# Kernel tuning notes

Hardware: AMD Instinct MI355X
Metric: run time of the kernel (lower is better)

The kernel has to match this reference:

```python
import jax, jax.numpy as jnp
import numpy as np

HIDDEN = 384
HEADS = 8
DIM_HEAD = HIDDEN // HEADS  # 48
INNER = DIM_HEAD * HEADS
SCALE = DIM_HEAD ** -0.5


def setup_inputs() -> dict:
    key = jax.random.key(0)
    k1, k2, k3, k4 = jax.random.split(key, 4)
    B, C, D, H, W = 2, HIDDEN, 16, 16, 8
    x = jax.random.normal(k1, (B, C, D, H, W), dtype=jnp.float32)
    # nn.Linear weights (stored as [out, in] in torch; use [in, out] here)
    w_qkv = jax.random.normal(k2, (C, 3 * INNER), dtype=jnp.float32) * (C ** -0.5)
    w_out = jax.random.normal(k3, (INNER, C), dtype=jnp.float32) * (INNER ** -0.5)
    b_out = jax.random.normal(k4, (C,), dtype=jnp.float32) * 0.02
    return {"x": x, "w_qkv": w_qkv, "w_out": w_out, "b_out": b_out}


def reference(x, w_qkv, w_out, b_out):
    B, C, D, H, W = x.shape
    N = D * H * W
    tokens = x.reshape(B, C, N).transpose(0, 2, 1)          # [B, N, C]
    qkv = tokens @ w_qkv                                     # [B, N, 3*inner]
    qkv = qkv.reshape(B, N, 3, HEADS, DIM_HEAD).transpose(2, 0, 3, 1, 4)
    q, k, v = qkv[0], qkv[1], qkv[2]                         # [B, h, N, dh]
    q = jnp.clip(q, -5.0, 5.0)
    k = jnp.clip(k, -5.0, 5.0)
    logits = jnp.einsum('bhnd,bhmd->bhnm', q, k) * SCALE     # [B, h, N, N]
    logits = logits - jnp.max(logits, axis=-1, keepdims=True)
    attn = jax.nn.softmax(logits, axis=-1)
    out = jnp.einsum('bhnm,bhmd->bhnd', attn, v)             # [B, h, N, dh]
    out = out.transpose(0, 2, 1, 3).reshape(B, N, INNER)     # [B, N, inner]
    out = out @ w_out + b_out                                # [B, N, C]
    out = out.transpose(0, 2, 1).reshape(B, C, D, H, W)
    return x + out
```

## Files before the change

### kernel.cpp

```cpp
#include <hip/hip_runtime.h>

#define B_SZ 2
#define C_IN 384
#define N_TOK 2048
#define HEADS 8
#define DH 48
#define J3 1152
#define ATTN_SCALE 0.14433756729740643f
#define KSPLIT 4
#define KEYS_PER_SPLIT 512

typedef __attribute__((ext_vector_type(8))) _Float16 f16x8;
typedef __attribute__((ext_vector_type(4))) _Float16 f16x4;
typedef __attribute__((ext_vector_type(4))) float f32x4;

__device__ __forceinline__ unsigned short f2h(float f) {
  _Float16 h = (_Float16)f;
  return __builtin_bit_cast(unsigned short, h);
}
__device__ __forceinline__ uint pk2(float a, float b) {
  return __builtin_bit_cast(uint, __builtin_amdgcn_cvt_pkrtz(a, b));
}

__global__ __launch_bounds__(256) void tr_kernel(
    const float* __restrict__ x, const float* __restrict__ wq,
    const float* __restrict__ wo, unsigned short* __restrict__ xh,
    unsigned short* __restrict__ wqh, unsigned short* __restrict__ woh) {
  const int z = blockIdx.z;
  const float* src;
  unsigned short* dst;
  int C;
  if (z < 2) {
    src = x + (size_t)z * C_IN * N_TOK;
    dst = xh + (size_t)z * N_TOK * C_IN;
    C = N_TOK;
  } else if (z == 2) {
    src = wq; dst = wqh; C = J3;
  } else {
    src = wo; dst = woh; C = C_IN;
  }
  const int c0 = blockIdx.x * 64;
  const int r0 = blockIdx.y * 64;
  if (c0 >= C) return;
  __shared__ unsigned short T[64][74];
  const int tid = threadIdx.x;
  const int cc = tid & 63;
#pragma unroll
  for (int i = 0; i < 16; ++i) {
    const int rr = 4 * i + (tid >> 6);
    T[cc][rr] = f2h(src[(size_t)(r0 + rr) * C + c0 + cc]);
  }
  __syncthreads();
  const int cc2 = tid >> 2;
  const int seg = (tid & 3) * 16;
  uint v[8];
#pragma unroll
  for (int k = 0; k < 8; ++k)
    v[k] = (uint)T[cc2][seg + 2 * k] | ((uint)T[cc2][seg + 2 * k + 1] << 16);
  unsigned short* dp = dst + (size_t)(c0 + cc2) * C_IN + r0 + seg;
  *(uint4*)dp = make_uint4(v[0], v[1], v[2], v[3]);
  *(uint4*)(dp + 8) = make_uint4(v[4], v[5], v[6], v[7]);
}

__global__ __launch_bounds__(256) void qkv_mfma(
    const unsigned short* __restrict__ xh, const unsigned short* __restrict__ wqh,
    unsigned short* __restrict__ Qo, unsigned short* __restrict__ Ko,
    unsigned short* __restrict__ Vo) {
  __shared__ __align__(16) unsigned short Ts[128][72];
  __shared__ __align__(16) unsigned short Ws[64][72];
  const int tid = threadIdx.x;
  const int w = tid >> 6, lane = tid & 63;
  const int lc = lane & 15, lg = lane >> 4;
  const int m0 = blockIdx.x * 128;
  const int j0 = blockIdx.y * 64;
  const int b = m0 >> 11;

  f32x4 acc[2][4];
#pragma unroll
  for (int i = 0; i < 2; ++i)
#pragma unroll
    for (int j = 0; j < 4; ++j) acc[i][j] = (f32x4){0.f, 0.f, 0.f, 0.f};

  const int trow = tid & 127, tseg = tid >> 7;
  const int wrow = tid & 63,  wseg = tid >> 6;

  for (int kk = 0; kk < C_IN; kk += 64) {
    {
      const uint4* s = (const uint4*)(xh + (size_t)(m0 + trow) * C_IN + kk + tseg * 32);
      uint4* d = (uint4*)&Ts[trow][tseg * 32];
      d[0] = s[0]; d[1] = s[1]; d[2] = s[2]; d[3] = s[3];
      const uint4* s2 = (const uint4*)(wqh + (size_t)(j0 + wrow) * C_IN + kk + wseg * 16);
      uint4* d2 = (uint4*)&Ws[wrow][wseg * 16];
      d2[0] = s2[0]; d2[1] = s2[1];
    }
    __syncthreads();
    f16x8 a[2][2], bf[4][2];
#pragma unroll
    for (int mt = 0; mt < 2; ++mt)
#pragma unroll
      for (int kh = 0; kh < 2; ++kh)
        a[mt][kh] = *(const f16x8*)&Ts[32 * w + 16 * mt + lc][32 * kh + 8 * lg];
#pragma unroll
    for (int jt = 0; jt < 4; ++jt)
#pragma unroll
      for (int kh = 0; kh < 2; ++kh)
        bf[jt][kh] = *(const f16x8*)&Ws[16 * jt + lc][32 * kh + 8 * lg];
#pragma unroll
    for (int mt = 0; mt < 2; ++mt)
#pragma unroll
      for (int jt = 0; jt < 4; ++jt)
#pragma unroll
        for (int kh = 0; kh < 2; ++kh)
          acc[mt][jt] = __builtin_amdgcn_mfma_f32_16x16x32_f16(a[mt][kh], bf[jt][kh], acc[mt][jt], 0, 0, 0);
    __syncthreads();
  }

#pragma unroll
  for (int jt = 0; jt < 4; ++jt) {
    const int jlo = j0 + 16 * jt;
    const int which = jlo / 384;
    const int rr = jlo - which * 384;
    const int head = rr / DH;
    const int dbase = rr - head * DH;
    const int d = dbase + lc;
    const int bh = b * HEADS + head;
#pragma unroll
    for (int mt = 0; mt < 2; ++mt)
#pragma unroll
      for (int r = 0; r < 4; ++r) {
        const int n = (m0 + 32 * w + 16 * mt + 4 * lg + r) & 2047;
        float val = acc[mt][jt][r];
        if (which == 0) {
          val = fminf(fmaxf(val, -5.f), 5.f) * ATTN_SCALE;
          Qo[((size_t)bh * N_TOK + n) * DH + d] = f2h(val);
        } else if (which == 1) {
          val = fminf(fmaxf(val, -5.f), 5.f);
          Ko[((size_t)bh * N_TOK + n) * DH + d] = f2h(val);
        } else {
          Vo[((size_t)bh * DH + d) * N_TOK + n] = f2h(val);
        }
      }
  }
}

__global__ __launch_bounds__(512) void attn_kernel(
    const unsigned short* __restrict__ Q, const unsigned short* __restrict__ K,
    const unsigned short* __restrict__ Vt, unsigned short* __restrict__ Opart,
    float2* __restrict__ ml) {
  const int qt = blockIdx.x, bh = blockIdx.y, ks = blockIdx.z;
  const int b = bh >> 3, h = bh & 7;
  const int n0 = qt * 128;
  const int tid = threadIdx.x;
  const int w = tid >> 6, lane = tid & 63;
  const int lc = lane & 15, lg = lane >> 4;

  __shared__ __align__(16) unsigned short Ks[2][64][56];
  __shared__ __align__(16) unsigned short Vs[2][48][68];

  const unsigned short* Qrow = Q + ((size_t)bh * N_TOK + n0 + 16 * w + lc) * DH;
  const f16x8 qf0 = *(const f16x8*)(Qrow + 8 * lg);
  f16x8 qf1 = {0, 0, 0, 0, 0, 0, 0, 0};
  {
    const f16x4 t = *(const f16x4*)(Qrow + 32 + 4 * lg);
    qf1[0] = t[0]; qf1[1] = t[1]; qf1[2] = t[2]; qf1[3] = t[3];
  }

  const unsigned short* Kg = K + (size_t)bh * N_TOK * DH + (size_t)ks * KEYS_PER_SPLIT * DH;
  const uint* Vg32 = (const uint*)(Vt + (size_t)bh * DH * N_TOK) + ks * (KEYS_PER_SPLIT / 2);

  uint kr[3], vr[3];
  auto issue = [&](int t0) {
    const uint* Ksrc = (const uint*)(Kg + (size_t)t0 * DH);
#pragma unroll
    for (int i = 0; i < 3; ++i) {
      const int dw = tid + i * 512;
      kr[i] = Ksrc[dw];
      vr[i] = Vg32[(size_t)(dw >> 5) * 1024 + (t0 >> 1) + (dw & 31)];
    }
  };
  auto commit = [&](int buf) {
#pragma unroll
    for (int i = 0; i < 3; ++i) {
      const int dw = tid + i * 512;
      const int key = dw / 24, c = dw - key * 24;
      *(uint*)&Ks[buf][key][2 * c] = kr[i];
      *(uint*)&Vs[buf][dw >> 5][2 * (dw & 31)] = vr[i];
    }
  };

  float m_run = -1e30f, l_run = 0.f;
  f32x4 oacc[3] = {{0,0,0,0},{0,0,0,0},{0,0,0,0}};

  issue(0);
  commit(0);

  for (int t = 0; t < KEYS_PER_SPLIT / 64; ++t) {
    const int cur = t & 1;
    if (t < KEYS_PER_SPLIT / 64 - 1) issue((t + 1) * 64);
    __syncthreads();

    f32x4 sac[4];
    __builtin_amdgcn_s_setprio(1);
#pragma unroll
    for (int it = 0; it < 4; ++it) {
      const int krow = 16 * it + lc;
      const f16x8 kf0 = *(const f16x8*)&Ks[cur][krow][8 * lg];
      f16x8 kf1 = {0, 0, 0, 0, 0, 0, 0, 0};
      const f16x4 tt = *(const f16x4*)&Ks[cur][krow][32 + 4 * lg];
      kf1[0] = tt[0]; kf1[1] = tt[1]; kf1[2] = tt[2]; kf1[3] = tt[3];
      const f32x4 z = {0.f, 0.f, 0.f, 0.f};
      f32x4 s = __builtin_amdgcn_mfma_f32_16x16x32_f16(kf0, qf0, z, 0, 0, 0);
      sac[it]  = __builtin_amdgcn_mfma_f32_16x16x32_f16(kf1, qf1, s, 0, 0, 0);
    }
    __builtin_amdgcn_s_setprio(0);

    float mt = -1e30f;
#pragma unroll
    for (int it = 0; it < 4; ++it)
#pragma unroll
      for (int r = 0; r < 4; ++r) mt = fmaxf(mt, sac[it][r]);
    mt = fmaxf(mt, __shfl_xor(mt, 16, 64));
    mt = fmaxf(mt, __shfl_xor(mt, 32, 64));
    const float mn = fmaxf(m_run, mt);
    const float rs = __expf(m_run - mn);
    m_run = mn;
    float p[4][4];
    float ps = 0.f;
#pragma unroll
    for (int it = 0; it < 4; ++it)
#pragma unroll
      for (int r = 0; r < 4; ++r) {
        p[it][r] = __expf(sac[it][r] - mn);
        ps += p[it][r];
      }
    ps += __shfl_xor(ps, 16, 64);
    ps += __shfl_xor(ps, 32, 64);
    l_run = l_run * rs + ps;
#pragma unroll
    for (int itd = 0; itd < 3; ++itd)
#pragma unroll
      for (int r = 0; r < 4; ++r) oacc[itd][r] *= rs;

    f16x8 pt[2];
#pragma unroll
    for (int ks2 = 0; ks2 < 2; ++ks2) {
      union { f16x8 v; uint u[4]; } pu;
      pu.u[0] = pk2(p[2 * ks2][0], p[2 * ks2][1]);
      pu.u[1] = pk2(p[2 * ks2][2], p[2 * ks2][3]);
      pu.u[2] = pk2(p[2 * ks2 + 1][0], p[2 * ks2 + 1][1]);
      pu.u[3] = pk2(p[2 * ks2 + 1][2], p[2 * ks2 + 1][3]);
      pt[ks2] = pu.v;
    }

    __builtin_amdgcn_s_setprio(1);
#pragma unroll
    for (int itd = 0; itd < 3; ++itd) {
      const int drow = 16 * itd + lc;
#pragma unroll
      for (int ks2 = 0; ks2 < 2; ++ks2) {
        const f16x4 v0 = *(const f16x4*)&Vs[cur][drow][4 * lg + 32 * ks2];
        const f16x4 v1 = *(const f16x4*)&Vs[cur][drow][4 * lg + 32 * ks2 + 16];
        f16x8 vf;
        vf[0] = v0[0]; vf[1] = v0[1]; vf[2] = v0[2]; vf[3] = v0[3];
        vf[4] = v1[0]; vf[5] = v1[1]; vf[6] = v1[2]; vf[7] = v1[3];
        oacc[itd] = __builtin_amdgcn_mfma_f32_16x16x32_f16(vf, pt[ks2], oacc[itd], 0, 0, 0);
      }
    }
    __builtin_amdgcn_s_setprio(0);

    if (t < KEYS_PER_SPLIT / 64 - 1) commit(cur ^ 1);
  }

  if (lg == 0)
    ml[(size_t)(ks * 16 + bh) * N_TOK + n0 + 16 * w + lc] = make_float2(m_run, l_run);
  unsigned short* Ap = Opart +
      ((size_t)(ks * B_SZ + b) * N_TOK + n0 + 16 * w + lc) * 384 + h * DH;
#pragma unroll
  for (int itd = 0; itd < 3; ++itd) {
    uint2 pkv;
    pkv.x = pk2(oacc[itd][0], oacc[itd][1]);
    pkv.y = pk2(oacc[itd][2], oacc[itd][3]);
    *(uint2*)(Ap + 16 * itd + 4 * lg) = pkv;
  }
}

__global__ __launch_bounds__(256) void combine_kernel(
    const unsigned short* __restrict__ Opart, const float2* __restrict__ ml,
    unsigned short* __restrict__ AOh) {
  const int vid = blockIdx.x * 256 + threadIdx.x;
  const int c8 = vid % 48;
  const int n  = (vid / 48) & 2047;
  const int b  = vid / (48 * 2048);
  const int c0 = c8 * 8;
  const int h  = c0 / 48;
  const int bh = b * 8 + h;
  const size_t PS = (size_t)B_SZ * N_TOK * 384;
  float2 e0 = ml[(size_t)(0 * 16 + bh) * N_TOK + n];
  float2 e1 = ml[(size_t)(1 * 16 + bh) * N_TOK + n];
  float2 e2 = ml[(size_t)(2 * 16 + bh) * N_TOK + n];
  float2 e3 = ml[(size_t)(3 * 16 + bh) * N_TOK + n];
  const float M = fmaxf(fmaxf(e0.x, e1.x), fmaxf(e2.x, e3.x));
  const float w0 = __expf(e0.x - M), w1 = __expf(e1.x - M);
  const float w2 = __expf(e2.x - M), w3 = __expf(e3.x - M);
  const float inv = 1.f / (w0 * e0.y + w1 * e1.y + w2 * e2.y + w3 * e3.y);
  const float s0 = w0 * inv, s1 = w1 * inv, s2 = w2 * inv, s3 = w3 * inv;
  const size_t o = ((size_t)b * N_TOK + n) * 384 + c0;
  union U8 { uint4 q; _Float16 e[8]; } u0, u1, u2, u3, r;
  u0.q = *(const uint4*)(Opart + 0 * PS + o);
  u1.q = *(const uint4*)(Opart + 1 * PS + o);
  u2.q = *(const uint4*)(Opart + 2 * PS + o);
  u3.q = *(const uint4*)(Opart + 3 * PS + o);
#pragma unroll
  for (int k = 0; k < 8; k += 2) {
    const float a = (float)u0.e[k] * s0 + (float)u1.e[k] * s1 +
                    (float)u2.e[k] * s2 + (float)u3.e[k] * s3;
    const float bb = (float)u0.e[k + 1] * s0 + (float)u1.e[k + 1] * s1 +
                     (float)u2.e[k + 1] * s2 + (float)u3.e[k + 1] * s3;
    *(uint*)&r.e[k] = pk2(a, bb);
  }
  *(uint4*)(AOh + o) = r.q;
}

__global__ __launch_bounds__(256) void proj_mfma(
    const unsigned short* __restrict__ AOh, const unsigned short* __restrict__ woh,
    const float* __restrict__ b_out, const float* __restrict__ x,
    float* __restrict__ out) {
  __shared__ __align__(16) unsigned short As[64][72];
  __shared__ __align__(16) unsigned short Bs[128][72];
  const int tid = threadIdx.x;
  const int w = tid >> 6, lane = tid & 63;
  const int lc = lane & 15, lg = lane >> 4;
  const int c0 = blockIdx.x * 64;
  const int m0 = blockIdx.y * 128;
  const int b = m0 >> 11;

  f32x4 acc[4][2];
#pragma unroll
  for (int i = 0; i < 4; ++i)
#pragma unroll
    for (int j = 0; j < 2; ++j) acc[i][j] = (f32x4){0.f, 0.f, 0.f, 0.f};

  const int arow = tid & 63,  aseg = tid >> 6;
  const int brow = tid & 127, bseg = tid >> 7;

  for (int kk = 0; kk < C_IN; kk += 64) {
    {
      const uint4* s = (const uint4*)(woh + (size_t)(c0 + arow) * C_IN + kk + aseg * 16);
      uint4* d = (uint4*)&As[arow][aseg * 16];
      d[0] = s[0]; d[1] = s[1];
      const uint4* s2 = (const uint4*)(AOh + (size_t)(m0 + brow) * C_IN + kk + bseg * 32);
      uint4* d2 = (uint4*)&Bs[brow][bseg * 32];
      d2[0] = s2[0]; d2[1] = s2[1]; d2[2] = s2[2]; d2[3] = s2[3];
    }
    __syncthreads();
    f16x8 a[4][2], bf[2][2];
#pragma unroll
    for (int ct = 0; ct < 4; ++ct)
#pragma unroll
      for (int kh = 0; kh < 2; ++kh)
        a[ct][kh] = *(const f16x8*)&As[16 * ct + lc][32 * kh + 8 * lg];
#pragma unroll
    for (int mt = 0; mt < 2; ++mt)
#pragma unroll
      for (int kh = 0; kh < 2; ++kh)
        bf[mt][kh] = *(const f16x8*)&Bs[32 * w + 16 * mt + lc][32 * kh + 8 * lg];
#pragma unroll
    for (int ct = 0; ct < 4; ++ct)
#pragma unroll
      for (int mt = 0; mt < 2; ++mt)
#pragma unroll
        for (int kh = 0; kh < 2; ++kh)
          acc[ct][mt] = __builtin_amdgcn_mfma_f32_16x16x32_f16(a[ct][kh], bf[mt][kh], acc[ct][mt], 0, 0, 0);
    __syncthreads();
  }

#pragma unroll
  for (int ct = 0; ct < 4; ++ct)
#pragma unroll
    for (int r = 0; r < 4; ++r) {
      const int c = c0 + 16 * ct + 4 * lg + r;
      const float bias = b_out[c];
#pragma unroll
      for (int mt = 0; mt < 2; ++mt) {
        const int n = (m0 + 32 * w + 16 * mt + lc) & 2047;
        const size_t off = ((size_t)b * C_IN + c) * N_TOK + n;
        out[off] = x[off] + bias + acc[ct][mt][r];
      }
    }
}

extern "C" void kernel_launch(void* const* d_in, const int* in_sizes, int n_in,
                              void* d_out, int out_size, void* d_ws, size_t ws_size,
                              hipStream_t stream) {
  const float* x     = (const float*)d_in[0];
  const float* w_qkv = (const float*)d_in[1];
  const float* w_out = (const float*)d_in[2];
  const float* b_out = (const float*)d_in[3];
  float* out = (float*)d_out;

  char* ws = (char*)d_ws;
  unsigned short* xh    = (unsigned short*)(ws);
  unsigned short* wqh   = (unsigned short*)(ws + 3145728);
  unsigned short* woh   = (unsigned short*)(ws + 4030464);
  unsigned short* Qb    = (unsigned short*)(ws + 4325376);
  unsigned short* Kb    = (unsigned short*)(ws + 7471104);
  unsigned short* Vb    = (unsigned short*)(ws + 10616832);
  unsigned short* Opart = (unsigned short*)(ws + 13762560);
  float2*         mlb   = (float2*)(ws + 26345472);
  unsigned short* AOh   = (unsigned short*)(ws + 27394048);

  tr_kernel<<<dim3(32, 6, 4), 256, 0, stream>>>(x, w_qkv, w_out, xh, wqh, woh);
  qkv_mfma<<<dim3(32, 18), 256, 0, stream>>>(xh, wqh, Qb, Kb, Vb);
  attn_kernel<<<dim3(16, 16, KSPLIT), 512, 0, stream>>>(Qb, Kb, Vb, Opart, mlb);
  combine_kernel<<<dim3(768), 256, 0, stream>>>(Opart, mlb, AOh);
  proj_mfma<<<dim3(6, 32), 256, 0, stream>>>(AOh, woh, b_out, x, out);
}
```

Before: 79.07 us.

## Use exp2 softmax with deferred rescale and coalesced V-transpose stores

```diff
diff --git a/kernel.cpp b/kernel.cpp
--- a/kernel.cpp
+++ b/kernel.cpp
@@ -6,9 +6,10 @@
 #define HEADS 8
 #define DH 48
 #define J3 1152
-#define ATTN_SCALE 0.14433756729740643f
+#define QSCALE_LOG2 0.20823509110768f
 #define KSPLIT 4
 #define KEYS_PER_SPLIT 512
+#define DEFER_THR 11.0f
 
 typedef __attribute__((ext_vector_type(8))) _Float16 f16x8;
 typedef __attribute__((ext_vector_type(4))) _Float16 f16x4;
@@ -20,6 +21,9 @@
 }
 __device__ __forceinline__ uint pk2(float a, float b) {
   return __builtin_bit_cast(uint, __builtin_amdgcn_cvt_pkrtz(a, b));
+}
+__device__ __forceinline__ float exp2g(float x) {
+  return __builtin_amdgcn_exp2f(x);
 }
 
 __global__ __launch_bounds__(256) void tr_kernel(
@@ -115,31 +119,53 @@
     __syncthreads();
   }
 
-#pragma unroll
-  for (int jt = 0; jt < 4; ++jt) {
-    const int jlo = j0 + 16 * jt;
-    const int which = jlo / 384;
-    const int rr = jlo - which * 384;
-    const int head = rr / DH;
-    const int dbase = rr - head * DH;
-    const int d = dbase + lc;
-    const int bh = b * HEADS + head;
-#pragma unroll
-    for (int mt = 0; mt < 2; ++mt)
-#pragma unroll
-      for (int r = 0; r < 4; ++r) {
-        const int n = (m0 + 32 * w + 16 * mt + 4 * lg + r) & 2047;
-        float val = acc[mt][jt][r];
-        if (which == 0) {
-          val = fminf(fmaxf(val, -5.f), 5.f) * ATTN_SCALE;
-          Qo[((size_t)bh * N_TOK + n) * DH + d] = f2h(val);
-        } else if (which == 1) {
-          val = fminf(fmaxf(val, -5.f), 5.f);
-          Ko[((size_t)bh * N_TOK + n) * DH + d] = f2h(val);
-        } else {
-          Vo[((size_t)bh * DH + d) * N_TOK + n] = f2h(val);
+  if (j0 >= 768) {
+    unsigned short* Tv = &Ts[0][0];
+#pragma unroll
+    for (int jt = 0; jt < 4; ++jt)
+#pragma unroll
+      for (int mt = 0; mt < 2; ++mt)
+#pragma unroll
+        for (int r = 0; r < 4; ++r)
+          Tv[(16 * jt + lc) * 136 + (32 * w + 16 * mt + 4 * lg + r)] =
+              f2h(acc[mt][jt][r]);
+    __syncthreads();
+    const int n0 = m0 & 2047;
+#pragma unroll
+    for (int i = 0; i < 4; ++i) {
+      const int s = tid + i * 256;
+      const int row = s >> 4;
+      const int segoff = (s & 15) * 8;
+      const int rr2 = j0 - 768 + row;
+      const int head = rr2 / DH;
+      const int d = rr2 - head * DH;
+      const int bh = b * HEADS + head;
+      *(uint4*)(Vo + ((size_t)bh * DH + d) * N_TOK + n0 + segoff) =
+          *(const uint4*)&Tv[row * 136 + segoff];
+    }
+  } else {
+#pragma unroll
+    for (int jt = 0; jt < 4; ++jt) {
+      const int jlo = j0 + 16 * jt;
+      const int which = jlo / 384;
+      const int rr = jlo - which * 384;
+      const int head = rr / DH;
+      const int dbase = rr - head * DH;
+      const int d = dbase + lc;
+      const int bh = b * HEADS + head;
+#pragma unroll
+      for (int mt = 0; mt < 2; ++mt)
+#pragma unroll
+        for (int r = 0; r < 4; ++r) {
+          const int n = (m0 + 32 * w + 16 * mt + 4 * lg + r) & 2047;
+          float val = fminf(fmaxf(acc[mt][jt][r], -5.f), 5.f);
+          if (which == 0) {
+            Qo[((size_t)bh * N_TOK + n) * DH + d] = f2h(val * QSCALE_LOG2);
+          } else {
+            Ko[((size_t)bh * N_TOK + n) * DH + d] = f2h(val);
+          }
         }
-      }
+    }
   }
 }
 
@@ -221,25 +247,30 @@
       for (int r = 0; r < 4; ++r) mt = fmaxf(mt, sac[it][r]);
     mt = fmaxf(mt, __shfl_xor(mt, 16, 64));
     mt = fmaxf(mt, __shfl_xor(mt, 32, 64));
-    const float mn = fmaxf(m_run, mt);
-    const float rs = __expf(m_run - mn);
-    m_run = mn;
+
+    if (!__all(mt - m_run <= DEFER_THR)) {
+      const float mn = fmaxf(m_run, mt);
+      const float rs = exp2g(m_run - mn);
+      m_run = mn;
+      l_run *= rs;
+#pragma unroll
+      for (int itd = 0; itd < 3; ++itd)
+#pragma unroll
+        for (int r = 0; r < 4; ++r) oacc[itd][r] *= rs;
+    }
+
     float p[4][4];
     float ps = 0.f;
 #pragma unroll
     for (int it = 0; it < 4; ++it)
 #pragma unroll
       for (int r = 0; r < 4; ++r) {
-        p[it][r] = __expf(sac[it][r] - mn);
+        p[it][r] = exp2g(sac[it][r] - m_run);
         ps += p[it][r];
       }
     ps += __shfl_xor(ps, 16, 64);
     ps += __shfl_xor(ps, 32, 64);
-    l_run = l_run * rs + ps;
-#pragma unroll
-    for (int itd = 0; itd < 3; ++itd)
-#pragma unroll
-      for (int r = 0; r < 4; ++r) oacc[itd][r] *= rs;
+    l_run += ps;
 
     f16x8 pt[2];
 #pragma unroll
@@ -273,13 +304,14 @@
 
   if (lg == 0)
     ml[(size_t)(ks * 16 + bh) * N_TOK + n0 + 16 * w + lc] = make_float2(m_run, l_run);
+  const float inv = 1.f / l_run;
   unsigned short* Ap = Opart +
       ((size_t)(ks * B_SZ + b) * N_TOK + n0 + 16 * w + lc) * 384 + h * DH;
 #pragma unroll
   for (int itd = 0; itd < 3; ++itd) {
     uint2 pkv;
-    pkv.x = pk2(oacc[itd][0], oacc[itd][1]);
-    pkv.y = pk2(oacc[itd][2], oacc[itd][3]);
+    pkv.x = pk2(oacc[itd][0] * inv, oacc[itd][1] * inv);
+    pkv.y = pk2(oacc[itd][2] * inv, oacc[itd][3] * inv);
     *(uint2*)(Ap + 16 * itd + 4 * lg) = pkv;
   }
 }
@@ -300,10 +332,10 @@
   float2 e2 = ml[(size_t)(2 * 16 + bh) * N_TOK + n];
   float2 e3 = ml[(size_t)(3 * 16 + bh) * N_TOK + n];
   const float M = fmaxf(fmaxf(e0.x, e1.x), fmaxf(e2.x, e3.x));
-  const float w0 = __expf(e0.x - M), w1 = __expf(e1.x - M);
-  const float w2 = __expf(e2.x - M), w3 = __expf(e3.x - M);
-  const float inv = 1.f / (w0 * e0.y + w1 * e1.y + w2 * e2.y + w3 * e3.y);
-  const float s0 = w0 * inv, s1 = w1 * inv, s2 = w2 * inv, s3 = w3 * inv;
+  const float g0 = exp2g(e0.x - M) * e0.y, g1 = exp2g(e1.x - M) * e1.y;
+  const float g2 = exp2g(e2.x - M) * e2.y, g3 = exp2g(e3.x - M) * e3.y;
+  const float inv = 1.f / (g0 + g1 + g2 + g3);
+  const float s0 = g0 * inv, s1 = g1 * inv, s2 = g2 * inv, s3 = g3 * inv;
   const size_t o = ((size_t)b * N_TOK + n) * 384 + c0;
   union U8 { uint4 q; _Float16 e[8]; } u0, u1, u2, u3, r;
   u0.q = *(const uint4*)(Opart + 0 * PS + o);
```

Result: faster. 75.22 us, median of 2 (-4.9%).
